# Kernel optimization log

Hardware: AMD Instinct MI355X
Metric: run time of the kernel (lower is better)

Reference implementation:

```python
import jax, jax.numpy as jnp
import numpy as np

C_OUT = 16
C_IN = 16
L0 = 64        # layer_sizes[0]
H = 128        # hidden width
D_IN = C_IN * L0  # 1024, flattened per-point input dim


def _uniform(key, shape, fan_in):
    bound = 1.0 / np.sqrt(fan_in)
    return jax.random.uniform(key, shape, jnp.float32, -bound, bound)


def setup_inputs() -> dict:
    key = jax.random.key(0)
    ks = jax.random.split(key, 7)
    x = jax.random.normal(ks[0], (65536, C_IN, L0), jnp.float32)
    # Stacked per-output-channel MLP weights (torch Linear transposed: [in, out])
    W1 = _uniform(ks[1], (C_OUT, D_IN, H), D_IN)
    b1 = _uniform(ks[2], (C_OUT, H), D_IN)
    W2 = _uniform(ks[3], (C_OUT, H, H), H)
    b2 = _uniform(ks[4], (C_OUT, H, H)[:2], H)
    W3 = _uniform(ks[5], (C_OUT, H, 1), H)
    b3 = _uniform(ks[6], (C_OUT, 1), H)
    return {"x": x, "W1": W1, "b1": b1, "W2": W2, "b2": b2, "W3": W3, "b3": b3}


def reference(x, W1, b1, W2, b2, W3, b3):
    # x: [N, C_in, L0] -> flatten per point to [N, D_IN]
    N = x.shape[0]
    xf = x.reshape(N, -1)
    # Batched per-output-channel GEMMs (replaces Python loop over channels_out)
    h = jax.nn.relu(jnp.einsum('nd,cdh->cnh', xf, W1) + b1[:, None, :])   # [C, N, H]
    h = jax.nn.relu(jnp.einsum('cnh,chk->cnk', h, W2) + b2[:, None, :])   # [C, N, H]
    out = jnp.einsum('cnh,cho->cno', h, W3) + b3[:, None, :]              # [C, N, 1]
    # squeeze(-1) then permute channel axis to the end: [N, C_out]
    return out[..., 0].T
```

## Files before the change

kernel.cpp:

```cpp
#include <hip/hip_runtime.h>
#include <cstdint>

typedef unsigned short u16;
typedef __attribute__((ext_vector_type(4))) float f32x4;
typedef __attribute__((ext_vector_type(8))) __bf16 bf16x8;
typedef __attribute__((ext_vector_type(8))) u16 u16x8;

#define C_OUT 16
#define D_IN 1024
#define HDIM 128
#define NPTS 65536
#define BN 128
#define BK 64

__device__ __forceinline__ u16 f2bf(float f){
  uint32_t u = __builtin_bit_cast(uint32_t, f);
  u += 0x7FFFu + ((u >> 16) & 1u);
  return (u16)(u >> 16);
}

__device__ __forceinline__ void gload_lds16(const void* g, void* l){
  __builtin_amdgcn_global_load_lds((const __attribute__((address_space(1))) void*)g,
                                   (__attribute__((address_space(3))) void*)l, 16, 0, 0);
}

__global__ __launch_bounds__(256) void transpose_cvt(const float* __restrict__ src,
                                                     u16* __restrict__ dst, int R, int C){
  __shared__ float tile[32][33];
  int ch = blockIdx.z;
  int r0 = blockIdx.y * 32, c0 = blockIdx.x * 32;
  const float* s = src + (size_t)ch * R * C;
  u16* d = dst + (size_t)ch * R * C;
  int tx = threadIdx.x, ty = threadIdx.y;
  for (int i = ty; i < 32; i += 8) tile[i][tx] = s[(size_t)(r0 + i) * C + c0 + tx];
  __syncthreads();
  for (int i = ty; i < 32; i += 8) d[(size_t)(c0 + i) * R + r0 + tx] = f2bf(tile[tx][i]);
}

__global__ __launch_bounds__(256, 3) void mlp_fused(const float* __restrict__ xf,
    const u16* __restrict__ W1T, const u16* __restrict__ W2T,
    const float* __restrict__ b1, const float* __restrict__ b2,
    const float* __restrict__ W3, const float* __restrict__ b3,
    float* __restrict__ out){
  __shared__ __align__(16) u16 smem[2 * BN * BK];
  __shared__ float outb[BN];
  u16* As = smem;
  u16* Bs = smem + BN * BK;

  const int t = threadIdx.x;
  const int wave = t >> 6, lane = t & 63;
  const int q = lane >> 4, s = lane & 15;
  const int wr = (wave >> 1) * 64, wc = (wave & 1) * 64;
  const int c = blockIdx.x & 15;
  const int n0 = (blockIdx.x >> 4) * BN;

  const u16* w1c = W1T + (size_t)c * HDIM * D_IN;

  f32x4 acc[4][4];
#pragma unroll
  for (int i = 0; i < 4; i++)
#pragma unroll
    for (int j = 0; j < 4; j++) acc[i][j] = (f32x4){0.f, 0.f, 0.f, 0.f};

  const int arow = t >> 3;
  const int alc  = t & 7;
  float4 pv0[4], pv1[4];
#pragma unroll
  for (int rr = 0; rr < 4; rr++){
    int row = rr * 32 + arow;
    const float* p = xf + (size_t)(n0 + row) * D_IN + alc * 8;
    pv0[rr] = *(const float4*)p;
    pv1[rr] = *(const float4*)(p + 4);
  }

  for (int kt = 0; kt < D_IN / BK; kt++){
#pragma unroll
    for (int ii = 0; ii < 4; ii++){
      int hbase = wave * 32 + ii * 8;
      int h = hbase + (lane >> 3);
      int k = kt * BK + (((lane & 7) ^ (h & 7)) * 8);
      gload_lds16(w1c + (size_t)h * D_IN + k, &Bs[hbase * BK]);
    }
#pragma unroll
    for (int rr = 0; rr < 4; rr++){
      int row = rr * 32 + arow;
      u16x8 pk = { f2bf(pv0[rr].x), f2bf(pv0[rr].y), f2bf(pv0[rr].z), f2bf(pv0[rr].w),
                   f2bf(pv1[rr].x), f2bf(pv1[rr].y), f2bf(pv1[rr].z), f2bf(pv1[rr].w) };
      int sc = alc ^ (row & 7);
      *(u16x8*)&As[row * BK + sc * 8] = pk;
    }
    __syncthreads();
    if (kt + 1 < D_IN / BK){
#pragma unroll
      for (int rr = 0; rr < 4; rr++){
        int row = rr * 32 + arow;
        const float* p = xf + (size_t)(n0 + row) * D_IN + (kt + 1) * BK + alc * 8;
        pv0[rr] = *(const float4*)p;
        pv1[rr] = *(const float4*)(p + 4);
      }
    }
#pragma unroll
    for (int ks = 0; ks < 2; ks++){
      bf16x8 a[4], b[4];
#pragma unroll
      for (int i = 0; i < 4; i++){
        int m = wr + i * 16 + s;
        int ch = ks * 4 + q;
        a[i] = __builtin_bit_cast(bf16x8, *(const u16x8*)&As[m * BK + ((ch ^ (m & 7)) * 8)]);
      }
#pragma unroll
      for (int j = 0; j < 4; j++){
        int hh = wc + j * 16 + s;
        int ch = ks * 4 + q;
        b[j] = __builtin_bit_cast(bf16x8, *(const u16x8*)&Bs[hh * BK + ((ch ^ (hh & 7)) * 8)]);
      }
#pragma unroll
      for (int i = 0; i < 4; i++)
#pragma unroll
        for (int j = 0; j < 4; j++)
          acc[i][j] = __builtin_amdgcn_mfma_f32_16x16x32_bf16(a[i], b[j], acc[i][j], 0, 0, 0);
    }
    __syncthreads();
  }

  float b1v[4];
#pragma unroll
  for (int j = 0; j < 4; j++) b1v[j] = b1[c * HDIM + wc + j * 16 + s];
  u16* h1s = smem;
#pragma unroll
  for (int i = 0; i < 4; i++)
#pragma unroll
    for (int j = 0; j < 4; j++)
#pragma unroll
      for (int r = 0; r < 4; r++){
        float v = fmaxf(acc[i][j][r] + b1v[j], 0.f);
        int m = wr + i * 16 + q * 4 + r;
        int h = wc + j * 16 + s;
        h1s[m * HDIM + (((h >> 3) ^ (m & 7)) * 8) + (h & 7)] = f2bf(v);
      }
  __syncthreads();

  const u16* w2c = W2T + (size_t)c * HDIM * HDIM;
  f32x4 acc2[4][4];
#pragma unroll
  for (int i = 0; i < 4; i++)
#pragma unroll
    for (int j = 0; j < 4; j++) acc2[i][j] = (f32x4){0.f, 0.f, 0.f, 0.f};
#pragma unroll
  for (int ks = 0; ks < 4; ks++){
    bf16x8 a[4], b[4];
#pragma unroll
    for (int i = 0; i < 4; i++){
      int m = wr + i * 16 + s;
      int ch = ks * 4 + q;
      a[i] = __builtin_bit_cast(bf16x8, *(const u16x8*)&h1s[m * HDIM + ((ch ^ (m & 7)) * 8)]);
    }
#pragma unroll
    for (int j = 0; j < 4; j++){
      int col = wc + j * 16 + s;
      b[j] = __builtin_bit_cast(bf16x8, *(const u16x8*)(w2c + (size_t)col * HDIM + ks * 32 + q * 8));
    }
#pragma unroll
    for (int i = 0; i < 4; i++)
#pragma unroll
      for (int j = 0; j < 4; j++)
        acc2[i][j] = __builtin_amdgcn_mfma_f32_16x16x32_bf16(a[i], b[j], acc2[i][j], 0, 0, 0);
  }

  float b2v[4], w3v[4];
#pragma unroll
  for (int j = 0; j < 4; j++){
    b2v[j] = b2[c * HDIM + wc + j * 16 + s];
    w3v[j] = W3[c * HDIM + wc + j * 16 + s];
  }
  float part[4][4];
#pragma unroll
  for (int i = 0; i < 4; i++)
#pragma unroll
    for (int r = 0; r < 4; r++) part[i][r] = 0.f;
#pragma unroll
  for (int i = 0; i < 4; i++)
#pragma unroll
    for (int j = 0; j < 4; j++)
#pragma unroll
      for (int r = 0; r < 4; r++){
        float hv = fmaxf(acc2[i][j][r] + b2v[j], 0.f);
        part[i][r] = fmaf(hv, w3v[j], part[i][r]);
      }
#pragma unroll
  for (int mask = 1; mask <= 8; mask <<= 1)
#pragma unroll
    for (int i = 0; i < 4; i++)
#pragma unroll
      for (int r = 0; r < 4; r++) part[i][r] += __shfl_xor(part[i][r], mask, 64);

  if (s == 0 && wc == 0){
#pragma unroll
    for (int i = 0; i < 4; i++)
#pragma unroll
      for (int r = 0; r < 4; r++) outb[wr + i * 16 + q * 4 + r] = part[i][r];
  }
  __syncthreads();
  if (s == 0 && wc == 64){
#pragma unroll
    for (int i = 0; i < 4; i++)
#pragma unroll
      for (int r = 0; r < 4; r++) outb[wr + i * 16 + q * 4 + r] += part[i][r];
  }
  __syncthreads();
  if (t < BN) out[(size_t)(n0 + t) * C_OUT + c] = outb[t] + b3[c];
}

__global__ __launch_bounds__(256) void mlp_naive(const float* __restrict__ x,
    const float* __restrict__ W1, const float* __restrict__ b1,
    const float* __restrict__ W2, const float* __restrict__ b2,
    const float* __restrict__ W3, const float* __restrict__ b3,
    float* __restrict__ out){
  __shared__ float xs[16 * D_IN];
  __shared__ float h1[16 * HDIM];
  __shared__ float h2[16 * HDIM];
  int c = blockIdx.x & 15;
  int n0 = (blockIdx.x >> 4) * 16;
  int t = threadIdx.x;
  for (int i = t; i < 16 * D_IN; i += 256) xs[i] = x[(size_t)n0 * D_IN + i];
  __syncthreads();
  int h = t & 127, ng = t >> 7;
  const float* w1c = W1 + (size_t)c * D_IN * HDIM;
  float a1[8];
#pragma unroll
  for (int nn = 0; nn < 8; nn++) a1[nn] = 0.f;
  for (int d = 0; d < D_IN; d++){
    float w = w1c[(size_t)d * HDIM + h];
#pragma unroll
    for (int nn = 0; nn < 8; nn++) a1[nn] = fmaf(xs[(ng * 8 + nn) * D_IN + d], w, a1[nn]);
  }
  float bb = b1[c * HDIM + h];
#pragma unroll
  for (int nn = 0; nn < 8; nn++) h1[(ng * 8 + nn) * HDIM + h] = fmaxf(a1[nn] + bb, 0.f);
  __syncthreads();
  const float* w2c = W2 + (size_t)c * HDIM * HDIM;
  float a2[8];
#pragma unroll
  for (int nn = 0; nn < 8; nn++) a2[nn] = 0.f;
  for (int k = 0; k < HDIM; k++){
    float w = w2c[(size_t)k * HDIM + h];
#pragma unroll
    for (int nn = 0; nn < 8; nn++) a2[nn] = fmaf(h1[(ng * 8 + nn) * HDIM + k], w, a2[nn]);
  }
  bb = b2[c * HDIM + h];
#pragma unroll
  for (int nn = 0; nn < 8; nn++) h2[(ng * 8 + nn) * HDIM + h] = fmaxf(a2[nn] + bb, 0.f);
  __syncthreads();
  if (t < 16){
    float ssum = 0.f;
    for (int hh = 0; hh < HDIM; hh++) ssum = fmaf(h2[t * HDIM + hh], W3[c * HDIM + hh], ssum);
    out[(size_t)(n0 + t) * C_OUT + c] = ssum + b3[c];
  }
}

extern "C" void kernel_launch(void* const* d_in, const int* in_sizes, int n_in,
                              void* d_out, int out_size, void* d_ws, size_t ws_size,
                              hipStream_t stream){
  const float* x  = (const float*)d_in[0];
  const float* W1 = (const float*)d_in[1];
  const float* b1 = (const float*)d_in[2];
  const float* W2 = (const float*)d_in[3];
  const float* b2 = (const float*)d_in[4];
  const float* W3 = (const float*)d_in[5];
  const float* b3 = (const float*)d_in[6];
  float* out = (float*)d_out;

  const size_t W1T_elems = (size_t)C_OUT * HDIM * D_IN;
  const size_t W2T_elems = (size_t)C_OUT * HDIM * HDIM;
  const size_t ws_w_bytes = (W1T_elems + W2T_elems) * 2;

  if (ws_size < ws_w_bytes){
    mlp_naive<<<(NPTS / 16) * C_OUT, 256, 0, stream>>>(x, W1, b1, W2, b2, W3, b3, out);
    return;
  }

  u16* W1T = (u16*)d_ws;
  u16* W2T = W1T + W1T_elems;
  transpose_cvt<<<dim3(HDIM / 32, D_IN / 32, C_OUT), dim3(32, 8), 0, stream>>>(W1, W1T, D_IN, HDIM);
  transpose_cvt<<<dim3(HDIM / 32, HDIM / 32, C_OUT), dim3(32, 8), 0, stream>>>(W2, W2T, HDIM, HDIM);

  const int grid = (NPTS / BN) * C_OUT;
  mlp_fused<<<grid, 256, 0, stream>>>(x, W1T, W2T, b1, b2, W3, b3, out);
}
```

Baseline: 744.1 us.

## Pre-convert x to bf16 and load A fragments directly from global memory

```diff
diff --git a/kernel.cpp b/kernel.cpp
--- a/kernel.cpp
+++ b/kernel.cpp
@@ -11,7 +11,7 @@
 #define HDIM 128
 #define NPTS 65536
 #define BN 128
-#define BK 64
+#define BK2 128
 
 __device__ __forceinline__ u16 f2bf(float f){
   uint32_t u = __builtin_bit_cast(uint32_t, f);
@@ -37,15 +37,26 @@
   for (int i = ty; i < 32; i += 8) d[(size_t)(c0 + i) * R + r0 + tx] = f2bf(tile[tx][i]);
 }
 
-__global__ __launch_bounds__(256, 3) void mlp_fused(const float* __restrict__ xf,
+__global__ __launch_bounds__(256) void cvt_x_kernel(const float4* __restrict__ src,
+                                                    u16x8* __restrict__ dst, int n8){
+  int stride = gridDim.x * 256;
+  for (int i = blockIdx.x * 256 + threadIdx.x; i < n8; i += stride){
+    float4 v0 = src[2 * i];
+    float4 v1 = src[2 * i + 1];
+    u16x8 o = { f2bf(v0.x), f2bf(v0.y), f2bf(v0.z), f2bf(v0.w),
+                f2bf(v1.x), f2bf(v1.y), f2bf(v1.z), f2bf(v1.w) };
+    dst[i] = o;
+  }
+}
+
+__global__ __launch_bounds__(256, 3) void mlp_fused(const u16* __restrict__ xb,
     const u16* __restrict__ W1T, const u16* __restrict__ W2T,
     const float* __restrict__ b1, const float* __restrict__ b2,
     const float* __restrict__ W3, const float* __restrict__ b3,
     float* __restrict__ out){
-  __shared__ __align__(16) u16 smem[2 * BN * BK];
+  __shared__ __align__(16) u16 smem[BN * BK2];
   __shared__ float outb[BN];
-  u16* As = smem;
-  u16* Bs = smem + BN * BK;
+  u16* Bs = smem;
 
   const int t = threadIdx.x;
   const int wave = t >> 6, lane = t & 63;
@@ -55,6 +66,9 @@
   const int n0 = (blockIdx.x >> 4) * BN;
 
   const u16* w1c = W1T + (size_t)c * HDIM * D_IN;
+  const u16* xrow[4];
+#pragma unroll
+  for (int i = 0; i < 4; i++) xrow[i] = xb + (size_t)(n0 + wr + i * 16 + s) * D_IN;
 
   f32x4 acc[4][4];
 #pragma unroll
@@ -62,66 +76,49 @@
 #pragma unroll
     for (int j = 0; j < 4; j++) acc[i][j] = (f32x4){0.f, 0.f, 0.f, 0.f};
 
-  const int arow = t >> 3;
-  const int alc  = t & 7;
-  float4 pv0[4], pv1[4];
-#pragma unroll
-  for (int rr = 0; rr < 4; rr++){
-    int row = rr * 32 + arow;
-    const float* p = xf + (size_t)(n0 + row) * D_IN + alc * 8;
-    pv0[rr] = *(const float4*)p;
-    pv1[rr] = *(const float4*)(p + 4);
-  }
-
-  for (int kt = 0; kt < D_IN / BK; kt++){
-#pragma unroll
-    for (int ii = 0; ii < 4; ii++){
-      int hbase = wave * 32 + ii * 8;
-      int h = hbase + (lane >> 3);
-      int k = kt * BK + (((lane & 7) ^ (h & 7)) * 8);
-      gload_lds16(w1c + (size_t)h * D_IN + k, &Bs[hbase * BK]);
-    }
-#pragma unroll
-    for (int rr = 0; rr < 4; rr++){
-      int row = rr * 32 + arow;
-      u16x8 pk = { f2bf(pv0[rr].x), f2bf(pv0[rr].y), f2bf(pv0[rr].z), f2bf(pv0[rr].w),
-                   f2bf(pv1[rr].x), f2bf(pv1[rr].y), f2bf(pv1[rr].z), f2bf(pv1[rr].w) };
-      int sc = alc ^ (row & 7);
-      *(u16x8*)&As[row * BK + sc * 8] = pk;
-    }
+  for (int kt2 = 0; kt2 < D_IN / BK2; kt2++){
     __syncthreads();
-    if (kt + 1 < D_IN / BK){
-#pragma unroll
-      for (int rr = 0; rr < 4; rr++){
-        int row = rr * 32 + arow;
-        const float* p = xf + (size_t)(n0 + row) * D_IN + (kt + 1) * BK + alc * 8;
-        pv0[rr] = *(const float4*)p;
-        pv1[rr] = *(const float4*)(p + 4);
-      }
-    }
-#pragma unroll
-    for (int ks = 0; ks < 2; ks++){
-      bf16x8 a[4], b[4];
-#pragma unroll
-      for (int i = 0; i < 4; i++){
-        int m = wr + i * 16 + s;
-        int ch = ks * 4 + q;
-        a[i] = __builtin_bit_cast(bf16x8, *(const u16x8*)&As[m * BK + ((ch ^ (m & 7)) * 8)]);
-      }
+#pragma unroll
+    for (int ii = 0; ii < 8; ii++){
+      int slot = ii * 256 + t;
+      int h = slot >> 4;
+      int pos = slot & 15;
+      int g = (pos & 8) | ((pos & 7) ^ (h & 7));
+      gload_lds16(w1c + (size_t)h * D_IN + kt2 * BK2 + g * 8,
+                  &Bs[(ii * 256 + wave * 64) * 8]);
+    }
+    __syncthreads();
+
+    u16x8 acur[4], anxt[4];
+#pragma unroll
+    for (int i = 0; i < 4; i++)
+      acur[i] = *(const u16x8*)(xrow[i] + kt2 * BK2 + q * 8);
+#pragma unroll
+    for (int ks = 0; ks < 4; ks++){
+      if (ks < 3){
+#pragma unroll
+        for (int i = 0; i < 4; i++)
+          anxt[i] = *(const u16x8*)(xrow[i] + kt2 * BK2 + (ks + 1) * 32 + q * 8);
+      }
+      bf16x8 b[4];
 #pragma unroll
       for (int j = 0; j < 4; j++){
         int hh = wc + j * 16 + s;
-        int ch = ks * 4 + q;
-        b[j] = __builtin_bit_cast(bf16x8, *(const u16x8*)&Bs[hh * BK + ((ch ^ (hh & 7)) * 8)]);
+        int l = ks * 4 + q;
+        int pos = (l & 8) | ((l & 7) ^ (hh & 7));
+        b[j] = __builtin_bit_cast(bf16x8, *(const u16x8*)&Bs[hh * BK2 + pos * 8]);
       }
 #pragma unroll
       for (int i = 0; i < 4; i++)
 #pragma unroll
         for (int j = 0; j < 4; j++)
-          acc[i][j] = __builtin_amdgcn_mfma_f32_16x16x32_bf16(a[i], b[j], acc[i][j], 0, 0, 0);
-    }
-    __syncthreads();
-  }
+          acc[i][j] = __builtin_amdgcn_mfma_f32_16x16x32_bf16(
+              __builtin_bit_cast(bf16x8, acur[i]), b[j], acc[i][j], 0, 0, 0);
+#pragma unroll
+      for (int i = 0; i < 4; i++) acur[i] = anxt[i];
+    }
+  }
+  __syncthreads();
 
   float b1v[4];
 #pragma unroll
@@ -272,18 +269,21 @@
 
   const size_t W1T_elems = (size_t)C_OUT * HDIM * D_IN;
   const size_t W2T_elems = (size_t)C_OUT * HDIM * HDIM;
-  const size_t ws_w_bytes = (W1T_elems + W2T_elems) * 2;
-
-  if (ws_size < ws_w_bytes){
+  const size_t xb_elems  = (size_t)NPTS * D_IN;
+  const size_t ws_bytes  = (W1T_elems + W2T_elems + xb_elems) * 2;
+
+  if (ws_size < ws_bytes){
     mlp_naive<<<(NPTS / 16) * C_OUT, 256, 0, stream>>>(x, W1, b1, W2, b2, W3, b3, out);
     return;
   }
 
   u16* W1T = (u16*)d_ws;
   u16* W2T = W1T + W1T_elems;
+  u16* xb  = W2T + W2T_elems;
   transpose_cvt<<<dim3(HDIM / 32, D_IN / 32, C_OUT), dim3(32, 8), 0, stream>>>(W1, W1T, D_IN, HDIM);
   transpose_cvt<<<dim3(HDIM / 32, HDIM / 32, C_OUT), dim3(32, 8), 0, stream>>>(W2, W2T, HDIM, HDIM);
+  cvt_x_kernel<<<8192, 256, 0, stream>>>((const float4*)x, (u16x8*)xb, (int)(xb_elems / 8));
 
   const int grid = (NPTS / BN) * C_OUT;
-  mlp_fused<<<grid, 256, 0, stream>>>(x, W1T, W2T, b1, b2, W3, b3, out);
-}
+  mlp_fused<<<grid, 256, 0, stream>>>(xb, W1T, W2T, b1, b2, W3, b3, out);
+}
```

New measurement: 1.046 ms. 1.41x slower.
